# Kernel optimization log

Measured on AMD Instinct MI355X. Metric: run time of the kernel, lower is better.

The kernel has to match this reference:

```python
import jax, jax.numpy as jnp
import numpy as np

B, N, D, H, T = 32, 4096, 256, 8, 28  # batch, nodes, hidden_dim, bottleneck_dim, horizon


def setup_inputs() -> dict:
    key = jax.random.key(0)
    ks = jax.random.split(key, 16)
    s = 0.1
    return {
        "x": jax.random.normal(ks[0], (B, N, D), jnp.float32),
        "last_step": jax.random.normal(ks[1], (B, N), jnp.float32),
        # GRU params (PyTorch layout: gates ordered r, z, n)
        "W_ih": jax.random.normal(ks[2], (3 * H, 1), jnp.float32) * s,
        "W_hh": jax.random.normal(ks[3], (3 * H, H), jnp.float32) * s,
        "b_ih": jax.random.normal(ks[4], (3 * H,), jnp.float32) * s,
        "b_hh": jax.random.normal(ks[5], (3 * H,), jnp.float32) * s,
        # hidden_proj: Linear(D -> H)
        "Wp": jax.random.normal(ks[6], (H, D), jnp.float32) * s,
        "bp": jax.random.normal(ks[7], (H,), jnp.float32) * s,
        # output_proj: Linear(H -> 1)
        "Wo": jax.random.normal(ks[8], (1, H), jnp.float32) * s,
        "bo": jax.random.normal(ks[9], (1,), jnp.float32) * s,
        # refine_gate: Linear(D->H), ReLU, Linear(H->T), Sigmoid
        "Wg1": jax.random.normal(ks[10], (H, D), jnp.float32) * s,
        "bg1": jax.random.normal(ks[11], (H,), jnp.float32) * s,
        "Wg2": jax.random.normal(ks[12], (T, H), jnp.float32) * s,
        "bg2": jax.random.normal(ks[13], (T,), jnp.float32) * s,
        "log_decay": jnp.float32(-2.3),
    }


def _rollout(x, last_step, W_ih, W_hh, b_ih, b_hh, Wp, bp, Wo, bo, Wg1, bg1, Wg2, bg2, log_decay):
    b, n, d = x.shape
    h = x.reshape(b * n, d) @ Wp.T + bp                 # [BN, H] initial GRU hidden
    cur = last_step.reshape(b * n)                       # scalar input per row
    w_ih = W_ih[:, 0]                                    # [3H] (input_size == 1)

    def step(carry, _):
        h, cur = carry
        gi = cur[:, None] * w_ih[None, :] + b_ih         # [BN, 3H]
        gh = h @ W_hh.T + b_hh                           # [BN, 3H]
        r = jax.nn.sigmoid(gi[:, :H] + gh[:, :H])
        z = jax.nn.sigmoid(gi[:, H:2 * H] + gh[:, H:2 * H])
        ncand = jnp.tanh(gi[:, 2 * H:] + r * gh[:, 2 * H:])
        h_new = (1.0 - z) * ncand + z * h
        pred = h_new @ Wo[0] + bo[0]                     # [BN]
        return (h_new, pred), pred

    (_, _), preds = jax.lax.scan(step, (h, cur), None, length=T)  # [T, BN]
    gru_pred = preds.T.reshape(b, n, T)                  # [B, N, T]

    gate = jax.nn.sigmoid(
        jax.nn.relu(jnp.einsum('bnd,hd->bnh', x, Wg1) + bg1) @ Wg2.T + bg2
    )                                                    # [B, N, T]
    time_steps = jnp.arange(1, T + 1, dtype=x.dtype)
    decay_curve = jnp.exp(-jnp.exp(log_decay) * time_steps)       # [T]
    decay_pred = last_step[..., None] * decay_curve               # [B, N, T]
    return gate * gru_pred + (1.0 - gate) * decay_pred


def reference(x, last_step, W_ih, W_hh, b_ih, b_hh, Wp, bp, Wo, bo, Wg1, bg1, Wg2, bg2, log_decay):
    return _rollout(x, last_step, W_ih, W_hh, b_ih, b_hh, Wp, bp, Wo, bo, Wg1, bg1, Wg2, bg2, log_decay)
```

## Files before the change

kernel.cpp:

```cpp
#include <hip/hip_runtime.h>

#define TT 28
#define L2E 1.4426950408889634f

typedef __attribute__((ext_vector_type(8))) short bf16x8;
typedef __attribute__((ext_vector_type(4))) float f32x4;
typedef _Float16 h2 __attribute__((ext_vector_type(2)));
typedef __fp16 fp16x2 __attribute__((ext_vector_type(2)));

__device__ __forceinline__ unsigned fbits(float f){ union{float f; unsigned u;} v; v.f=f; return v.u; }
__device__ __forceinline__ float bitsf(unsigned u){ union{unsigned u; float f;} v; v.u=u; return v.f; }
__device__ __forceinline__ short bf16rnd(float f){ return (short)((fbits(f)+0x8000u)>>16); }

__device__ __forceinline__ h2 PKH2(float a, float b){
    fp16x2 t = __builtin_amdgcn_cvt_pkrtz(a, b);
    return __builtin_bit_cast(h2, t);
}

#if __has_builtin(__builtin_amdgcn_fdot2)
#define FDOT2(a,b,c) __builtin_amdgcn_fdot2((a),(b),(c),false)
#else
__device__ __forceinline__ float FDOT2(h2 a, h2 b, float c){
    return fmaf((float)a.x,(float)b.x, fmaf((float)a.y,(float)b.y,(c)));
}
#endif
#if __has_builtin(__builtin_amdgcn_exp2f)
#define EXP2(x) __builtin_amdgcn_exp2f(x)
#else
#define EXP2(x) exp2f(x)
#endif
#if __has_builtin(__builtin_amdgcn_rcpf)
#define RCP(x) __builtin_amdgcn_rcpf(x)
#else
#define RCP(x) (1.f/(x))
#endif

#if __has_builtin(__builtin_amdgcn_mov_dpp)
#define DPP_XOR1(x) __builtin_bit_cast(float, __builtin_amdgcn_mov_dpp(__builtin_bit_cast(int,(float)(x)), 0xB1, 0xF, 0xF, true))
#define DPP_XOR2(x) __builtin_bit_cast(float, __builtin_amdgcn_mov_dpp(__builtin_bit_cast(int,(float)(x)), 0x4E, 0xF, 0xF, true))
#else
#define DPP_XOR1(x) __shfl_xor((x), 1, 64)
#define DPP_XOR2(x) __shfl_xor((x), 2, 64)
#endif

__global__ __launch_bounds__(256) __attribute__((amdgpu_waves_per_eu(5, 8)))
void horizon_kernel(
    const float* __restrict__ x, const float* __restrict__ last_step,
    const float* __restrict__ W_ih, const float* __restrict__ W_hh,
    const float* __restrict__ b_ih, const float* __restrict__ b_hh,
    const float* __restrict__ Wp, const float* __restrict__ bp,
    const float* __restrict__ Wo, const float* __restrict__ bo,
    const float* __restrict__ Wg1, const float* __restrict__ bg1,
    const float* __restrict__ Wg2, const float* __restrict__ bg2,
    const float* __restrict__ log_decay, float* __restrict__ out)
{
    __shared__ __attribute__((aligned(16))) float s_whh[24*8];
    __shared__ __attribute__((aligned(16))) float s_wih[24];
    __shared__ __attribute__((aligned(16))) float s_b1[16];
    __shared__ __attribute__((aligned(16))) float s_bin[8];
    __shared__ __attribute__((aligned(16))) float s_bhn[8];
    __shared__ __attribute__((aligned(16))) float s_wo[8];
    __shared__ __attribute__((aligned(16))) float s_gw[28*8];
    __shared__ __attribute__((aligned(16))) float s_gb[28];
    __shared__ __attribute__((aligned(16))) float s_park[64][17];

    const int tid = threadIdx.x;

    if (tid < 192) s_whh[tid] = W_hh[tid] * (tid < 128 ? L2E : 2.0f*L2E);
    if (tid < 224) s_gw[tid]  = Wg2[tid] * L2E;
    if (tid < 28)  s_gb[tid]  = bg2[tid] * L2E;
    if (tid < 24)  s_wih[tid] = W_ih[tid] * (tid < 16 ? L2E : 2.0f*L2E);
    if (tid < 16)  s_b1[tid]  = (b_ih[tid] + b_hh[tid]) * L2E;
    if (tid < 8){
        s_bin[tid] = b_ih[16+tid] * (2.0f*L2E);
        s_bhn[tid] = b_hh[16+tid] * (2.0f*L2E);
        s_wo[tid]  = Wo[tid];
    }
    __syncthreads();

    const int lane = tid & 63;
    const int wv   = tid >> 6;
    const int c    = lane >> 4;
    const int rl   = lane & 15;
    const int rowBase = blockIdx.x * 64;

    {
        const float* wrow = (rl < 8) ? (Wp + rl*256) : (Wg1 + (rl-8)*256);
        bf16x8 bfrag[8];
        #pragma unroll
        for (int kk=0; kk<8; ++kk){
            #pragma unroll
            for (int j=0; j<8; ++j) bfrag[kk][j] = bf16rnd(wrow[kk*32 + c*8 + j]);
        }
        const float aBias = (rl < 8) ? bp[rl] : bg1[rl-8];
        const float* xrow = x + (size_t)(rowBase + wv*16 + rl) * 256;
        f32x4 acc = {0.f, 0.f, 0.f, 0.f};
        #pragma unroll
        for (int kk=0; kk<8; ++kk){
            float4 v0 = *(const float4*)(xrow + kk*32 + c*8);
            float4 v1 = *(const float4*)(xrow + kk*32 + c*8 + 4);
            float xs[8] = {v0.x,v0.y,v0.z,v0.w, v1.x,v1.y,v1.z,v1.w};
            bf16x8 ahi, alo;
            #pragma unroll
            for (int j=0; j<8; ++j){
                unsigned u  = fbits(xs[j]);
                unsigned hb = (u + 0x8000u) & 0xFFFF0000u;
                ahi[j] = (short)(hb >> 16);
                alo[j] = bf16rnd(xs[j] - bitsf(hb));
            }
            acc = __builtin_amdgcn_mfma_f32_16x16x32_bf16(ahi, bfrag[kk], acc, 0, 0, 0);
            acc = __builtin_amdgcn_mfma_f32_16x16x32_bf16(alo, bfrag[kk], acc, 0, 0, 0);
        }
        #pragma unroll
        for (int r=0; r<4; ++r){
            float v = acc[r] + aBias;
            if (rl >= 8) v = fmaxf(v, 0.f);
            s_park[wv*16 + c*4 + r][rl] = v;
        }
    }

    const int row = tid >> 2;
    const int o   = tid & 3;
    const int rowG = rowBase + row;
    const int dd0 = o, dd1 = o^1, dd2 = o^2, dd3 = o^3;

    float harr[8];
    harr[0]=s_park[row][dd0]; harr[1]=s_park[row][dd1]; harr[2]=s_park[row][dd2]; harr[3]=s_park[row][dd3];
    harr[4]=s_park[row][4+dd0]; harr[5]=s_park[row][4+dd1]; harr[6]=s_park[row][4+dd2]; harr[7]=s_park[row][4+dd3];
    float hOwn0 = harr[0], hOwn1 = harr[4];
    h2 hh[4] = { PKH2(harr[0],harr[1]), PKH2(harr[2],harr[3]),
                 PKH2(harr[4],harr[5]), PKH2(harr[6],harr[7]) };

    const int rws[6] = { o, o+4, 8+o, 12+o, 16+o, 20+o };
    h2 wk[6][4];
    #pragma unroll
    for (int rr=0; rr<6; ++rr){
        const float* wp_ = &s_whh[rws[rr]*8];
        wk[rr][0] = PKH2(wp_[dd0], wp_[dd1]); wk[rr][1] = PKH2(wp_[dd2], wp_[dd3]);
        wk[rr][2] = PKH2(wp_[4+dd0], wp_[4+dd1]); wk[rr][3] = PKH2(wp_[4+dd2], wp_[4+dd3]);
    }
    const float w_r0 = s_wih[o],    w_r1 = s_wih[o+4];
    const float w_z0 = s_wih[8+o],  w_z1 = s_wih[12+o];
    const float w_n0 = s_wih[16+o], w_n1 = s_wih[20+o];
    const float b_r0 = s_b1[o],   b_r1 = s_b1[o+4];
    const float b_z0 = s_b1[8+o], b_z1 = s_b1[12+o];
    const float b_in0 = s_bin[o], b_in1 = s_bin[o+4];
    const float b_hn0 = s_bhn[o], b_hn1 = s_bhn[o+4];
    h2 wo2[4] = { PKH2(s_wo[dd0], s_wo[dd1]), PKH2(s_wo[dd2], s_wo[dd3]),
                  PKH2(s_wo[4+dd0], s_wo[4+dd1]), PKH2(s_wo[4+dd2], s_wo[4+dd3]) };

    float qv[8];
    #pragma unroll
    for (int j=0; j<8; ++j) qv[j] = s_park[row][8+j];
    float gates[7];
    #pragma unroll
    for (int i=0; i<7; ++i){
        const int t = 4*i + o;
        const float* gw = &s_gw[t*8];
        float gl = s_gb[t];
        #pragma unroll
        for (int j=0; j<8; ++j) gl = fmaf(gw[j], qv[j], gl);
        gates[i] = RCP(1.f + EXP2(-gl));
    }

    const float ls0 = last_step[rowG];
    const float boS = bo[0];
    float cur = ls0;
    float preds[7];

    #pragma unroll
    for (int t=0; t<TT; ++t){
        float sr0 = fmaf(cur, w_r0, b_r0), sr1 = fmaf(cur, w_r1, b_r1);
        float sz0 = fmaf(cur, w_z0, b_z0), sz1 = fmaf(cur, w_z1, b_z1);
        float gn0 = b_hn0, gn1 = b_hn1;
        #pragma unroll
        for (int k=0; k<4; ++k){
            sr0 = FDOT2(hh[k], wk[0][k], sr0);
            sr1 = FDOT2(hh[k], wk[1][k], sr1);
            sz0 = FDOT2(hh[k], wk[2][k], sz0);
            sz1 = FDOT2(hh[k], wk[3][k], sz1);
            gn0 = FDOT2(hh[k], wk[4][k], gn0);
            gn1 = FDOT2(hh[k], wk[5][k], gn1);
        }
        float r0 = RCP(1.f + EXP2(-sr0)), r1 = RCP(1.f + EXP2(-sr1));
        float e0 = EXP2(fmaf(r0, gn0, fmaf(cur, w_n0, b_in0)));
        float e1 = EXP2(fmaf(r1, gn1, fmaf(cur, w_n1, b_in1)));
        float nn0 = fmaf(-2.f, RCP(e0 + 1.f), 1.f);
        float nn1 = fmaf(-2.f, RCP(e1 + 1.f), 1.f);
        float z0 = RCP(1.f + EXP2(-sz0)), z1 = RCP(1.f + EXP2(-sz1));
        hOwn0 = fmaf(z0, hOwn0 - nn0, nn0);
        hOwn1 = fmaf(z1, hOwn1 - nn1, nn1);

        float a0 = DPP_XOR1(hOwn0), a1 = DPP_XOR1(hOwn1);
        float u0 = DPP_XOR2(hOwn0), u1 = DPP_XOR2(a0);
        float u2 = DPP_XOR2(hOwn1), u3 = DPP_XOR2(a1);
        hh[0] = PKH2(hOwn0, a0); hh[1] = PKH2(u0, u1);
        hh[2] = PKH2(hOwn1, a1); hh[3] = PKH2(u2, u3);

        float p = boS;
        #pragma unroll
        for (int k=0; k<4; ++k) p = FDOT2(hh[k], wo2[k], p);
        preds[t>>2] = ((t & 3) == o) ? p : preds[t>>2];
        cur = p;
    }

    const float lam = EXP2(log_decay[0] * L2E);
    const float c1  = -lam * L2E;
    float* orow = out + (size_t)rowG * TT;
    #pragma unroll
    for (int i=0; i<7; ++i){
        const int t = 4*i + o;
        float dp = ls0 * EXP2(c1 * (float)(t+1));
        orow[t] = fmaf(gates[i], preds[i] - dp, dp);
    }
}

extern "C" void kernel_launch(void* const* d_in, const int* in_sizes, int n_in,
                              void* d_out, int out_size, void* d_ws, size_t ws_size,
                              hipStream_t stream)
{
    const float* x         = (const float*)d_in[0];
    const float* last_step = (const float*)d_in[1];
    const float* W_ih      = (const float*)d_in[2];
    const float* W_hh      = (const float*)d_in[3];
    const float* b_ih      = (const float*)d_in[4];
    const float* b_hh      = (const float*)d_in[5];
    const float* Wp        = (const float*)d_in[6];
    const float* bp        = (const float*)d_in[7];
    const float* Wo        = (const float*)d_in[8];
    const float* bo        = (const float*)d_in[9];
    const float* Wg1       = (const float*)d_in[10];
    const float* bg1       = (const float*)d_in[11];
    const float* Wg2       = (const float*)d_in[12];
    const float* bg2       = (const float*)d_in[13];
    const float* log_decay = (const float*)d_in[14];

    hipLaunchKernelGGL(horizon_kernel, dim3(2048), dim3(256), 0, stream,
                       x, last_step, W_ih, W_hh, b_ih, b_hh, Wp, bp, Wo, bo,
                       Wg1, bg1, Wg2, bg2, log_decay, (float*)d_out);
}
```

Before: 234.2 us.

## Split fused kernel into projection kernel and GRU rollout kernel via workspace

```diff
diff --git a/kernel.cpp b/kernel.cpp
--- a/kernel.cpp
+++ b/kernel.cpp
@@ -44,13 +44,58 @@
 #endif
 
 __global__ __launch_bounds__(256) __attribute__((amdgpu_waves_per_eu(5, 8)))
-void horizon_kernel(
-    const float* __restrict__ x, const float* __restrict__ last_step,
+void phaseA_kernel(const float* __restrict__ x,
+                   const float* __restrict__ Wp,  const float* __restrict__ bp,
+                   const float* __restrict__ Wg1, const float* __restrict__ bg1,
+                   float* __restrict__ hq)
+{
+    const int tid  = threadIdx.x;
+    const int lane = tid & 63;
+    const int wv   = tid >> 6;
+    const int c    = lane >> 4;
+    const int rl   = lane & 15;
+    const int rowBase = blockIdx.x*64 + wv*16;
+
+    const float* wrow = (rl < 8) ? (Wp + rl*256) : (Wg1 + (rl-8)*256);
+    bf16x8 bfrag[8];
+    #pragma unroll
+    for (int kk=0; kk<8; ++kk){
+        #pragma unroll
+        for (int j=0; j<8; ++j) bfrag[kk][j] = bf16rnd(wrow[kk*32 + c*8 + j]);
+    }
+    const float aBias = (rl < 8) ? bp[rl] : bg1[rl-8];
+
+    const float* xrow = x + (size_t)(rowBase + rl) * 256;
+    f32x4 acc = {0.f, 0.f, 0.f, 0.f};
+    #pragma unroll
+    for (int kk=0; kk<8; ++kk){
+        float4 v0 = *(const float4*)(xrow + kk*32 + c*8);
+        float4 v1 = *(const float4*)(xrow + kk*32 + c*8 + 4);
+        float xs[8] = {v0.x,v0.y,v0.z,v0.w, v1.x,v1.y,v1.z,v1.w};
+        bf16x8 ahi, alo;
+        #pragma unroll
+        for (int j=0; j<8; ++j){
+            unsigned u  = fbits(xs[j]);
+            unsigned hb = (u + 0x8000u) & 0xFFFF0000u;
+            ahi[j] = (short)(hb >> 16);
+            alo[j] = bf16rnd(xs[j] - bitsf(hb));
+        }
+        acc = __builtin_amdgcn_mfma_f32_16x16x32_bf16(ahi, bfrag[kk], acc, 0, 0, 0);
+        acc = __builtin_amdgcn_mfma_f32_16x16x32_bf16(alo, bfrag[kk], acc, 0, 0, 0);
+    }
+    #pragma unroll
+    for (int r=0; r<4; ++r){
+        float v = acc[r] + aBias;
+        if (rl >= 8) v = fmaxf(v, 0.f);
+        hq[(size_t)(rowBase + c*4 + r)*16 + rl] = v;
+    }
+}
+
+__global__ __launch_bounds__(256) __attribute__((amdgpu_waves_per_eu(4, 8)))
+void phaseB_kernel(const float* __restrict__ hq, const float* __restrict__ last_step,
     const float* __restrict__ W_ih, const float* __restrict__ W_hh,
     const float* __restrict__ b_ih, const float* __restrict__ b_hh,
-    const float* __restrict__ Wp, const float* __restrict__ bp,
-    const float* __restrict__ Wo, const float* __restrict__ bo,
-    const float* __restrict__ Wg1, const float* __restrict__ bg1,
+    const float* __restrict__ Wo,  const float* __restrict__ bo,
     const float* __restrict__ Wg2, const float* __restrict__ bg2,
     const float* __restrict__ log_decay, float* __restrict__ out)
 {
@@ -62,10 +107,8 @@
     __shared__ __attribute__((aligned(16))) float s_wo[8];
     __shared__ __attribute__((aligned(16))) float s_gw[28*8];
     __shared__ __attribute__((aligned(16))) float s_gb[28];
-    __shared__ __attribute__((aligned(16))) float s_park[64][17];
 
     const int tid = threadIdx.x;
-
     if (tid < 192) s_whh[tid] = W_hh[tid] * (tid < 128 ? L2E : 2.0f*L2E);
     if (tid < 224) s_gw[tid]  = Wg2[tid] * L2E;
     if (tid < 28)  s_gb[tid]  = bg2[tid] * L2E;
@@ -78,65 +121,26 @@
     }
     __syncthreads();
 
-    const int lane = tid & 63;
-    const int wv   = tid >> 6;
-    const int c    = lane >> 4;
-    const int rl   = lane & 15;
-    const int rowBase = blockIdx.x * 64;
-
-    {
-        const float* wrow = (rl < 8) ? (Wp + rl*256) : (Wg1 + (rl-8)*256);
-        bf16x8 bfrag[8];
-        #pragma unroll
-        for (int kk=0; kk<8; ++kk){
-            #pragma unroll
-            for (int j=0; j<8; ++j) bfrag[kk][j] = bf16rnd(wrow[kk*32 + c*8 + j]);
-        }
-        const float aBias = (rl < 8) ? bp[rl] : bg1[rl-8];
-        const float* xrow = x + (size_t)(rowBase + wv*16 + rl) * 256;
-        f32x4 acc = {0.f, 0.f, 0.f, 0.f};
-        #pragma unroll
-        for (int kk=0; kk<8; ++kk){
-            float4 v0 = *(const float4*)(xrow + kk*32 + c*8);
-            float4 v1 = *(const float4*)(xrow + kk*32 + c*8 + 4);
-            float xs[8] = {v0.x,v0.y,v0.z,v0.w, v1.x,v1.y,v1.z,v1.w};
-            bf16x8 ahi, alo;
-            #pragma unroll
-            for (int j=0; j<8; ++j){
-                unsigned u  = fbits(xs[j]);
-                unsigned hb = (u + 0x8000u) & 0xFFFF0000u;
-                ahi[j] = (short)(hb >> 16);
-                alo[j] = bf16rnd(xs[j] - bitsf(hb));
-            }
-            acc = __builtin_amdgcn_mfma_f32_16x16x32_bf16(ahi, bfrag[kk], acc, 0, 0, 0);
-            acc = __builtin_amdgcn_mfma_f32_16x16x32_bf16(alo, bfrag[kk], acc, 0, 0, 0);
-        }
-        #pragma unroll
-        for (int r=0; r<4; ++r){
-            float v = acc[r] + aBias;
-            if (rl >= 8) v = fmaxf(v, 0.f);
-            s_park[wv*16 + c*4 + r][rl] = v;
-        }
-    }
-
-    const int row = tid >> 2;
-    const int o   = tid & 3;
-    const int rowG = rowBase + row;
+    const int row  = tid >> 2;
+    const int o    = tid & 3;
+    const int rowG = blockIdx.x*64 + row;
     const int dd0 = o, dd1 = o^1, dd2 = o^2, dd3 = o^3;
 
-    float harr[8];
-    harr[0]=s_park[row][dd0]; harr[1]=s_park[row][dd1]; harr[2]=s_park[row][dd2]; harr[3]=s_park[row][dd3];
-    harr[4]=s_park[row][4+dd0]; harr[5]=s_park[row][4+dd1]; harr[6]=s_park[row][4+dd2]; harr[7]=s_park[row][4+dd3];
-    float hOwn0 = harr[0], hOwn1 = harr[4];
-    h2 hh[4] = { PKH2(harr[0],harr[1]), PKH2(harr[2],harr[3]),
-                 PKH2(harr[4],harr[5]), PKH2(harr[6],harr[7]) };
+    const float4* hv = (const float4*)(hq + (size_t)rowG * 16);
+    float4 p0 = hv[0], p1 = hv[1], p2 = hv[2], p3 = hv[3];
+    float hf[8] = {p0.x,p0.y,p0.z,p0.w, p1.x,p1.y,p1.z,p1.w};
+    float qv[8] = {p2.x,p2.y,p2.z,p2.w, p3.x,p3.y,p3.z,p3.w};
+
+    float hOwn0 = hf[dd0], hOwn1 = hf[4+dd0];
+    h2 hh[4] = { PKH2(hf[dd0],hf[dd1]),     PKH2(hf[dd2],hf[dd3]),
+                 PKH2(hf[4+dd0],hf[4+dd1]), PKH2(hf[4+dd2],hf[4+dd3]) };
 
     const int rws[6] = { o, o+4, 8+o, 12+o, 16+o, 20+o };
     h2 wk[6][4];
     #pragma unroll
     for (int rr=0; rr<6; ++rr){
         const float* wp_ = &s_whh[rws[rr]*8];
-        wk[rr][0] = PKH2(wp_[dd0], wp_[dd1]); wk[rr][1] = PKH2(wp_[dd2], wp_[dd3]);
+        wk[rr][0] = PKH2(wp_[dd0], wp_[dd1]);     wk[rr][1] = PKH2(wp_[dd2], wp_[dd3]);
         wk[rr][2] = PKH2(wp_[4+dd0], wp_[4+dd1]); wk[rr][3] = PKH2(wp_[4+dd2], wp_[4+dd3]);
     }
     const float w_r0 = s_wih[o],    w_r1 = s_wih[o+4];
@@ -146,12 +150,9 @@
     const float b_z0 = s_b1[8+o], b_z1 = s_b1[12+o];
     const float b_in0 = s_bin[o], b_in1 = s_bin[o+4];
     const float b_hn0 = s_bhn[o], b_hn1 = s_bhn[o+4];
-    h2 wo2[4] = { PKH2(s_wo[dd0], s_wo[dd1]), PKH2(s_wo[dd2], s_wo[dd3]),
+    h2 wo2[4] = { PKH2(s_wo[dd0], s_wo[dd1]),     PKH2(s_wo[dd2], s_wo[dd3]),
                   PKH2(s_wo[4+dd0], s_wo[4+dd1]), PKH2(s_wo[4+dd2], s_wo[4+dd3]) };
 
-    float qv[8];
-    #pragma unroll
-    for (int j=0; j<8; ++j) qv[j] = s_park[row][8+j];
     float gates[7];
     #pragma unroll
     for (int i=0; i<7; ++i){
@@ -234,8 +235,11 @@
     const float* Wg2       = (const float*)d_in[12];
     const float* bg2       = (const float*)d_in[13];
     const float* log_decay = (const float*)d_in[14];
-
-    hipLaunchKernelGGL(horizon_kernel, dim3(2048), dim3(256), 0, stream,
-                       x, last_step, W_ih, W_hh, b_ih, b_hh, Wp, bp, Wo, bo,
-                       Wg1, bg1, Wg2, bg2, log_decay, (float*)d_out);
-}
+    float* hq = (float*)d_ws;
+
+    hipLaunchKernelGGL(phaseA_kernel, dim3(2048), dim3(256), 0, stream,
+                       x, Wp, bp, Wg1, bg1, hq);
+    hipLaunchKernelGGL(phaseB_kernel, dim3(2048), dim3(256), 0, stream,
+                       hq, last_step, W_ih, W_hh, b_ih, b_hh, Wo, bo,
+                       Wg2, bg2, log_decay, (float*)d_out);
+}
```

Result: slower. 262.8 us (+12.2%).
